# Kernel optimization log

Measured on AMD Instinct MI355X. Metric: run time of the kernel, lower is better.

Reference implementation:

```python
import jax, jax.numpy as jnp
import numpy as np

N_HASHES = 8
Q_ATTN = 128   # q_attn_size == q_cluster_size
K_ATTN = 128   # k_attn_size == k_cluster_size


def _lsh_positions(queries, keys, alpha, beta):
    """XBOX+ asymmetric transform followed by E2LSH hashing; returns sorted
    positions (cluster assignment = contiguous chunks of the sorted order).
    Mirrors torch's no_grad block: outputs are int indices."""
    q_norms = jnp.linalg.norm(queries, axis=-1, keepdims=True)          # [B,S,1]
    k_norms = jnp.linalg.norm(keys, axis=-1, keepdims=True)
    M = jnp.maximum(q_norms.max(axis=1, keepdims=True),
                    k_norms.max(axis=1, keepdims=True))                 # [B,1,1]
    q_ext = jnp.sqrt(jnp.maximum(M ** 2 - q_norms ** 2, 0.0))
    k_ext = jnp.sqrt(jnp.maximum(M ** 2 - k_norms ** 2, 0.0))
    Q = jnp.concatenate([queries, q_ext, jnp.zeros_like(q_ext)], axis=-1)  # [B,S,d+2]
    K = jnp.concatenate([keys, jnp.zeros_like(k_ext), k_ext], axis=-1)
    # E2LSH: (x @ a + b) / r with r = 1; argsort is invariant to the /r rescale
    q_hash = jnp.einsum('bsd,dh->hbs', Q, alpha) + beta[:, None, None]  # [H,B,S]
    k_hash = jnp.einsum('bsd,dh->hbs', K, alpha) + beta[:, None, None]
    return jnp.argsort(q_hash, axis=-1), jnp.argsort(k_hash, axis=-1)


def _smyrf_attention(queries, keys, values, q_pos, k_pos):
    H = q_pos.shape[0]
    bs, q_len, dim = queries.shape
    v_dim = values.shape[-1]
    nc = q_len // Q_ATTN  # num clusters

    def gather(x, pos):  # x: [B,S,D], pos: [H,B,S] -> [H,B,S,D]
        return jnp.take_along_axis(jnp.broadcast_to(x[None], (H,) + x.shape),
                                   pos[..., None], axis=2)

    sq = gather(queries, q_pos).reshape(H, bs, nc, Q_ATTN, dim)
    sk = gather(keys,    k_pos).reshape(H, bs, nc, K_ATTN, dim)
    sv = gather(values,  k_pos).reshape(H, bs, nc, K_ATTN, v_dim)

    # per-cluster attention (norm_factor = 1, matching the torch default)
    inner = jnp.einsum('hbcqd,hbckd->hbcqk', sq, sk)
    lse = jax.nn.logsumexp(inner, axis=-1, keepdims=True)
    dots = jnp.exp(inner - lse)
    bo = jnp.einsum('hbcqk,hbckv->hbcqv', dots, sv).reshape(H, bs, q_len, v_dim)

    # scatter back to original query order
    q_rev = jnp.argsort(q_pos, axis=-1)                                  # [H,B,S]
    o = jnp.take_along_axis(bo, q_rev[..., None], axis=2)                # [H,B,S,V]
    logits = jnp.take_along_axis(lse.reshape(H, bs, q_len), q_rev, axis=2)
    # combine hash rounds: softmax over the hash axis weighted by per-round lse
    probs = jnp.exp(logits - jax.nn.logsumexp(logits, axis=0, keepdims=True))
    return jnp.sum(o * probs[..., None], axis=0)                         # [B,S,V]


def setup_inputs() -> dict:
    key = jax.random.key(0)
    kq, kk, kv, ka, kb = jax.random.split(key, 5)
    bs, seqlen, dim = 16, 4096, 64
    queries = jax.random.normal(kq, (bs, seqlen, dim), dtype=jnp.float32)
    keys = jax.random.normal(kk, (bs, seqlen, dim), dtype=jnp.float32)
    values = jax.random.normal(kv, (bs, seqlen, dim), dtype=jnp.float32)
    alpha = jax.random.normal(ka, (dim + 2, N_HASHES), dtype=jnp.float32)
    beta = jax.random.uniform(kb, (N_HASHES,), dtype=jnp.float32)  # U(0, r=1)
    return {"queries": queries, "keys": keys, "values": values,
            "alpha": alpha, "beta": beta}


def reference(queries, keys, values, alpha, beta):
    q_pos, k_pos = _lsh_positions(queries, keys, alpha, beta)
    return _smyrf_attention(queries, keys, values, q_pos, k_pos)
```

## Files before the change

### kernel.cpp

```cpp
#include <hip/hip_runtime.h>
#include <hip/hip_bf16.h>

#define BS 16
#define SEQ 4096
#define DIM 64
#define NH 8
#define CL 128
#define NC (SEQ/CL)
#define NPAIR (NH*BS)
#define QS2 72
#define VS2 136
#define PS 72

typedef __attribute__((ext_vector_type(8))) short bf8_t;
typedef __attribute__((ext_vector_type(4))) float f4_t;

__device__ __forceinline__ unsigned short f2bf(float x) {
    union { float f; unsigned u; } a; a.f = x;
    unsigned r = a.u + 0x7FFF + ((a.u >> 16) & 1);
    return (unsigned short)(r >> 16);
}
__device__ __forceinline__ float bf2f(unsigned short h) {
    union { unsigned u; float f; } a; a.u = ((unsigned)h) << 16; return a.f;
}
__device__ __forceinline__ void split8(float4 a, float4 b, bf8_t& hi, bf8_t& lo) {
    float v[8] = {a.x, a.y, a.z, a.w, b.x, b.y, b.z, b.w};
    #pragma unroll
    for (int j = 0; j < 8; ++j) {
        unsigned short h = f2bf(v[j]);
        hi[j] = (short)h;
        lo[j] = (short)f2bf(v[j] - bf2f(h));
    }
}

__global__ __launch_bounds__(256) void norms_kernel(const float* __restrict__ q,
        const float* __restrict__ k, float* __restrict__ qn2, float* __restrict__ kn2,
        unsigned int* __restrict__ M2bits) {
    int blk = blockIdx.x;
    const int qblocks = BS*SEQ/64;
    bool is_q = blk < qblocks;
    int rowbase = (is_q ? blk : blk - qblocks) * 64;
    const float* src = is_q ? q : k;
    float* dst = is_q ? qn2 : kn2;
    int t = threadIdx.x;
    int sub = t & 3;
    int r = rowbase + (t >> 2);
    const float4* row4 = (const float4*)(src + (size_t)r*DIM) + sub*4;
    float s = 0.f;
    #pragma unroll
    for (int c2 = 0; c2 < 4; ++c2) {
        float4 vv = row4[c2];
        s += vv.x*vv.x + vv.y*vv.y + vv.z*vv.z + vv.w*vv.w;
    }
    s += __shfl_xor(s, 1);
    s += __shfl_xor(s, 2);
    if (sub == 0) dst[r] = s;
    __shared__ float red[256];
    red[t] = s;
    __syncthreads();
    #pragma unroll
    for (int o = 128; o > 0; o >>= 1) {
        if (t < o) red[t] = fmaxf(red[t], red[t + o]);
        __syncthreads();
    }
    if (t == 0) atomicMax(&M2bits[r / SEQ], __float_as_uint(red[0]));
}

__global__ __launch_bounds__(256) void hash_kernel(const float* __restrict__ q,
        const float* __restrict__ k, const float* __restrict__ qn2,
        const float* __restrict__ kn2, const unsigned int* __restrict__ M2bits,
        const float* __restrict__ alpha, const float* __restrict__ beta,
        float* __restrict__ qh, float* __restrict__ kh) {
    int t = threadIdx.x;
    int sub = t & 3;
    int r = blockIdx.x * 64 + (t >> 2);
    const float4* q4 = (const float4*)(q + (size_t)r*DIM) + sub*4;
    const float4* k4 = (const float4*)(k + (size_t)r*DIM) + sub*4;
    float qa[NH], ka[NH];
    #pragma unroll
    for (int h = 0; h < NH; ++h) { qa[h] = 0.f; ka[h] = 0.f; }
    #pragma unroll
    for (int c2 = 0; c2 < 4; ++c2) {
        int d0 = sub*16 + c2*4;
        float4 qv = q4[c2], kv = k4[c2];
        #pragma unroll
        for (int h = 0; h < NH; ++h) {
            float a0 = alpha[(d0+0)*NH+h], a1 = alpha[(d0+1)*NH+h];
            float a2 = alpha[(d0+2)*NH+h], a3 = alpha[(d0+3)*NH+h];
            qa[h] += qv.x*a0 + qv.y*a1 + qv.z*a2 + qv.w*a3;
            ka[h] += kv.x*a0 + kv.y*a1 + kv.z*a2 + kv.w*a3;
        }
    }
    #pragma unroll
    for (int h = 0; h < NH; ++h) {
        qa[h] += __shfl_xor(qa[h], 1); qa[h] += __shfl_xor(qa[h], 2);
        ka[h] += __shfl_xor(ka[h], 1); ka[h] += __shfl_xor(ka[h], 2);
    }
    if (sub == 0) {
        int b = r / SEQ;
        float m2 = __uint_as_float(M2bits[b]);
        float qe = sqrtf(fmaxf(m2 - qn2[r], 0.f));
        float ke = sqrtf(fmaxf(m2 - kn2[r], 0.f));
        #pragma unroll
        for (int h = 0; h < NH; ++h) {
            qh[(size_t)h*BS*SEQ + r] = qa[h] + qe*alpha[DIM*NH + h] + beta[h];
            kh[(size_t)h*BS*SEQ + r] = ka[h] + ke*alpha[(DIM+1)*NH + h] + beta[h];
        }
    }
}

__global__ __launch_bounds__(512) void sort_kernel(const float* __restrict__ qh,
        const float* __restrict__ kh, int* __restrict__ qpos, int* __restrict__ kpos) {
    __shared__ float sh[SEQ];
    __shared__ int si[SEQ];
    int blk = blockIdx.x;
    const float* src; int* dst;
    if (blk < NPAIR) { src = qh + (size_t)blk*SEQ; dst = qpos + (size_t)blk*SEQ; }
    else { src = kh + (size_t)(blk - NPAIR)*SEQ; dst = kpos + (size_t)(blk - NPAIR)*SEQ; }
    int t = threadIdx.x;
    for (int i = t; i < SEQ; i += 512) { sh[i] = src[i]; si[i] = i; }
    __syncthreads();
    for (int kk = 2; kk <= SEQ; kk <<= 1) {
        for (int j = kk >> 1; j > 0; j >>= 1) {
            #pragma unroll
            for (int w = 0; w < SEQ/512; ++w) {
                int i = t + w*512;
                int ixj = i ^ j;
                if (ixj > i) {
                    bool up = (i & kk) == 0;
                    float h1 = sh[i], h2 = sh[ixj];
                    int i1 = si[i], i2 = si[ixj];
                    bool gt = (h1 > h2) || (h1 == h2 && i1 > i2);
                    if (gt == up) { sh[i] = h2; sh[ixj] = h1; si[i] = i2; si[ixj] = i1; }
                }
            }
            __syncthreads();
        }
    }
    for (int i = t; i < SEQ; i += 512) dst[i] = si[i];
}

__global__ __launch_bounds__(512, 6) void lse_kernel(const float* __restrict__ q,
        const float* __restrict__ k, const int* __restrict__ qpos,
        const int* __restrict__ kpos, float* __restrict__ lse) {
    extern __shared__ char smem[];
    short* khi = (short*)smem;
    short* klo = khi + 128*QS2;
    int* qp = (int*)(smem + 36864);
    int* kp = qp + CL;
    int blk = blockIdx.x;
    int c = blk & (NC-1);
    int hb = blk / NC;
    int b = hb & (BS-1);
    int t = threadIdx.x, lane = t & 63, w = t >> 6;
    int l15 = lane & 15, lg = lane >> 4;
    size_t posbase = (size_t)hb*SEQ + (size_t)c*CL;

    int qrow = qpos[posbase + w*16 + l15];
    const float* qsrc = q + ((size_t)b*SEQ + qrow)*DIM + lg*8;
    float4 qv0 = *(const float4*)(qsrc);
    float4 qv1 = *(const float4*)(qsrc + 4);
    float4 qv2 = *(const float4*)(qsrc + 32);
    float4 qv3 = *(const float4*)(qsrc + 36);

    if (t < CL) qp[t] = qpos[posbase + t];
    else if (t < 2*CL) kp[t - CL] = kpos[posbase + (t - CL)];
    __syncthreads();
    for (int task = t; task < 2048; task += 512) {
        int r = task >> 4, d4 = task & 15;
        float4 vv = ((const float4*)(k + ((size_t)b*SEQ + kp[r])*DIM))[d4];
        ushort4 h, l;
        h.x = f2bf(vv.x); h.y = f2bf(vv.y); h.z = f2bf(vv.z); h.w = f2bf(vv.w);
        l.x = f2bf(vv.x - bf2f(h.x)); l.y = f2bf(vv.y - bf2f(h.y));
        l.z = f2bf(vv.z - bf2f(h.z)); l.w = f2bf(vv.w - bf2f(h.w));
        *(ushort4*)(khi + r*QS2 + d4*4) = h;
        *(ushort4*)(klo + r*QS2 + d4*4) = l;
    }
    bf8_t ah[2], al[2];
    split8(qv0, qv1, ah[0], al[0]);
    split8(qv2, qv3, ah[1], al[1]);
    __syncthreads();
    f4_t acc[8] = {};
    #pragma unroll
    for (int ks = 0; ks < 2; ++ks) {
        #pragma unroll
        for (int ct = 0; ct < 8; ++ct) {
            int brow = (ct*16 + l15)*QS2 + lg*8 + 32*ks;
            bf8_t bh = *(bf8_t*)(khi + brow);
            bf8_t bl = *(bf8_t*)(klo + brow);
            acc[ct] = __builtin_amdgcn_mfma_f32_16x16x32_bf16(ah[ks], bh, acc[ct], 0, 0, 0);
            acc[ct] = __builtin_amdgcn_mfma_f32_16x16x32_bf16(al[ks], bh, acc[ct], 0, 0, 0);
            acc[ct] = __builtin_amdgcn_mfma_f32_16x16x32_bf16(ah[ks], bl, acc[ct], 0, 0, 0);
        }
    }
    #pragma unroll
    for (int r = 0; r < 4; ++r) {
        float m = acc[0][r];
        #pragma unroll
        for (int ct = 1; ct < 8; ++ct) m = fmaxf(m, acc[ct][r]);
        m = fmaxf(m, __shfl_xor(m, 1)); m = fmaxf(m, __shfl_xor(m, 2));
        m = fmaxf(m, __shfl_xor(m, 4)); m = fmaxf(m, __shfl_xor(m, 8));
        float s = 0.f;
        #pragma unroll
        for (int ct = 0; ct < 8; ++ct) s += __expf(acc[ct][r] - m);
        s += __shfl_xor(s, 1); s += __shfl_xor(s, 2);
        s += __shfl_xor(s, 4); s += __shfl_xor(s, 8);
        if (l15 == 0) lse[(size_t)hb*SEQ + qp[w*16 + lg*4 + r]] = m + __logf(s);
    }
}

__global__ __launch_bounds__(256) void z_kernel(const float* __restrict__ lse,
        float* __restrict__ Z) {
    int i = blockIdx.x * 256 + threadIdx.x;
    float vals[NH];
    float m = -1e30f;
    #pragma unroll
    for (int h = 0; h < NH; ++h) {
        vals[h] = lse[(size_t)h*BS*SEQ + i];
        m = fmaxf(m, vals[h]);
    }
    float s = 0.f;
    #pragma unroll
    for (int h = 0; h < NH; ++h) s += expf(vals[h] - m);
    Z[i] = m + logf(s);
}

__global__ __launch_bounds__(512, 6) void attn_kernel(const float* __restrict__ q,
        const float* __restrict__ k, const float* __restrict__ v,
        const int* __restrict__ qpos, const int* __restrict__ kpos,
        const float* __restrict__ Z, float* __restrict__ out) {
    extern __shared__ char smem[];
    short* khi = (short*)smem;
    short* klo = khi + 128*QS2;
    short* vt = (short*)smem;
    short* pb = (short*)(smem + 17408);
    int* qp = (int*)(smem + 36864);
    int* kp = qp + CL;
    float* zq = (float*)(kp + CL);
    int blk = blockIdx.x;
    int c = blk & (NC-1);
    int hb = blk / NC;
    int b = hb & (BS-1);
    int t = threadIdx.x, lane = t & 63, w = t >> 6;
    int l15 = lane & 15, lg = lane >> 4;
    size_t posbase = (size_t)hb*SEQ + (size_t)c*CL;

    int qrow = qpos[posbase + w*16 + l15];
    const float* qsrc = q + ((size_t)b*SEQ + qrow)*DIM + lg*8;
    float4 qv0 = *(const float4*)(qsrc);
    float4 qv1 = *(const float4*)(qsrc + 4);
    float4 qv2 = *(const float4*)(qsrc + 32);
    float4 qv3 = *(const float4*)(qsrc + 36);

    if (t < CL) qp[t] = qpos[posbase + t];
    else if (t < 2*CL) kp[t - CL] = kpos[posbase + (t - CL)];
    __syncthreads();
    if (t < CL) zq[t] = Z[(size_t)b*SEQ + qp[t]];
    for (int task = t; task < 2048; task += 512) {
        int r = task >> 4, d4 = task & 15;
        float4 vv = ((const float4*)(k + ((size_t)b*SEQ + kp[r])*DIM))[d4];
        ushort4 h, l;
        h.x = f2bf(vv.x); h.y = f2bf(vv.y); h.z = f2bf(vv.z); h.w = f2bf(vv.w);
        l.x = f2bf(vv.x - bf2f(h.x)); l.y = f2bf(vv.y - bf2f(h.y));
        l.z = f2bf(vv.z - bf2f(h.z)); l.w = f2bf(vv.w - bf2f(h.w));
        *(ushort4*)(khi + r*QS2 + d4*4) = h;
        *(ushort4*)(klo + r*QS2 + d4*4) = l;
    }
    bf8_t ah[2], al[2];
    split8(qv0, qv1, ah[0], al[0]);
    split8(qv2, qv3, ah[1], al[1]);
    __syncthreads();
    f4_t acc[8] = {};
    #pragma unroll
    for (int ks = 0; ks < 2; ++ks) {
        #pragma unroll
        for (int ct = 0; ct < 8; ++ct) {
            int brow = (ct*16 + l15)*QS2 + lg*8 + 32*ks;
            bf8_t bh = *(bf8_t*)(khi + brow);
            bf8_t bl = *(bf8_t*)(klo + brow);
            acc[ct] = __builtin_amdgcn_mfma_f32_16x16x32_bf16(ah[ks], bh, acc[ct], 0, 0, 0);
            acc[ct] = __builtin_amdgcn_mfma_f32_16x16x32_bf16(al[ks], bh, acc[ct], 0, 0, 0);
            acc[ct] = __builtin_amdgcn_mfma_f32_16x16x32_bf16(ah[ks], bl, acc[ct], 0, 0, 0);
        }
    }
    {
        float zr[4];
        #pragma unroll
        for (int r = 0; r < 4; ++r) zr[r] = zq[w*16 + lg*4 + r];
        #pragma unroll
        for (int ct = 0; ct < 8; ++ct)
            #pragma unroll
            for (int r = 0; r < 4; ++r)
                acc[ct][r] = __expf(acc[ct][r] - zr[r]);
    }
    __syncthreads();
    float vr0[8], vr1[8];
    #pragma unroll
    for (int j = 0; j < 8; ++j) {
        int r0 = kp[w*8 + j];
        int r1 = kp[(w+8)*8 + j];
        vr0[j] = v[((size_t)b*SEQ + r0)*DIM + lane];
        vr1[j] = v[((size_t)b*SEQ + r1)*DIM + lane];
    }
    #pragma unroll
    for (int ct = 0; ct < 4; ++ct)
        #pragma unroll
        for (int r = 0; r < 4; ++r)
            pb[(w*16 + lg*4 + r)*PS + ct*16 + l15] = (short)f2bf(acc[ct][r]);
    {
        bf8_t pk0, pk1;
        #pragma unroll
        for (int j = 0; j < 8; ++j) { pk0[j] = (short)f2bf(vr0[j]); pk1[j] = (short)f2bf(vr1[j]); }
        *(bf8_t*)(vt + lane*VS2 + w*8)     = pk0;
        *(bf8_t*)(vt + lane*VS2 + (w+8)*8) = pk1;
    }
    __syncthreads();
    f4_t oacc[4] = {};
    #pragma unroll
    for (int ks = 0; ks < 2; ++ks) {
        bf8_t pa = *(bf8_t*)(pb + (w*16 + l15)*PS + ks*32 + lg*8);
        #pragma unroll
        for (int n = 0; n < 4; ++n) {
            bf8_t vb = *(bf8_t*)(vt + (n*16 + l15)*VS2 + ks*32 + lg*8);
            oacc[n] = __builtin_amdgcn_mfma_f32_16x16x32_bf16(pa, vb, oacc[n], 0, 0, 0);
        }
    }
    __syncthreads();
    #pragma unroll
    for (int ct = 4; ct < 8; ++ct)
        #pragma unroll
        for (int r = 0; r < 4; ++r)
            pb[(w*16 + lg*4 + r)*PS + (ct-4)*16 + l15] = (short)f2bf(acc[ct][r]);
    __syncthreads();
    #pragma unroll
    for (int ks = 2; ks < 4; ++ks) {
        bf8_t pa = *(bf8_t*)(pb + (w*16 + l15)*PS + (ks-2)*32 + lg*8);
        #pragma unroll
        for (int n = 0; n < 4; ++n) {
            bf8_t vb = *(bf8_t*)(vt + (n*16 + l15)*VS2 + ks*32 + lg*8);
            oacc[n] = __builtin_amdgcn_mfma_f32_16x16x32_bf16(pa, vb, oacc[n], 0, 0, 0);
        }
    }
    #pragma unroll
    for (int n = 0; n < 4; ++n)
        #pragma unroll
        for (int r = 0; r < 4; ++r) {
            int row = w*16 + lg*4 + r;
            atomicAdd(out + ((size_t)b*SEQ + qp[row])*DIM + n*16 + l15, oacc[n][r]);
        }
}

extern "C" void kernel_launch(void* const* d_in, const int* in_sizes, int n_in,
                              void* d_out, int out_size, void* d_ws, size_t ws_size,
                              hipStream_t stream) {
    const float* q     = (const float*)d_in[0];
    const float* k     = (const float*)d_in[1];
    const float* v     = (const float*)d_in[2];
    const float* alpha = (const float*)d_in[3];
    const float* beta  = (const float*)d_in[4];
    float* out = (float*)d_out;

    float* ws   = (float*)d_ws;
    float* M2   = ws;
    float* qn2  = ws + 64;
    float* kn2  = qn2 + BS*SEQ;
    float* qh   = kn2 + BS*SEQ;
    float* kh   = qh + (size_t)NH*BS*SEQ;
    int*   qpos = (int*)(kh + (size_t)NH*BS*SEQ);
    int*   kpos = qpos + (size_t)NH*BS*SEQ;
    float* lse  = (float*)(kpos + (size_t)NH*BS*SEQ);
    float* Z    = lse + (size_t)NH*BS*SEQ;

    hipMemsetAsync(M2, 0, 64*sizeof(float), stream);
    hipMemsetAsync(out, 0, (size_t)out_size*sizeof(float), stream);

    norms_kernel<<<2*BS*SEQ/64, 256, 0, stream>>>(q, k, qn2, kn2, (unsigned int*)M2);
    hash_kernel<<<BS*SEQ/64, 256, 0, stream>>>(q, k, qn2, kn2, (const unsigned int*)M2,
                                               alpha, beta, qh, kh);
    sort_kernel<<<2*NPAIR, 512, 0, stream>>>(qh, kh, qpos, kpos);

    const int lse_lds  = 36864 + 2*CL*(int)sizeof(int);
    const int attn_lds = 36864 + 2*CL*(int)sizeof(int) + CL*(int)sizeof(float);
    lse_kernel<<<NH*BS*NC, 512, lse_lds, stream>>>(q, k, qpos, kpos, lse);
    z_kernel<<<BS*SEQ/256, 256, 0, stream>>>(lse, Z);
    attn_kernel<<<NH*BS*NC, 512, attn_lds, stream>>>(q, k, v, qpos, kpos, Z, out);
}
```

Measured before the change: 392.0 us.

## Bitonic sort: handle small-stride stages in registers with 1024 threads

The bitonic sort kernel now gives each thread 4 contiguous elements and runs the compare-exchange steps with stride below 4 in registers. This removes two shared-memory passes and two barriers per merge stage, plus the initial stages. The block size also doubles to 1024 threads, and loads and stores use vectorised float4/int4 accesses. The larger-stride stages still go through shared memory. The bigger block may limit how many blocks run per CU.

```diff
diff --git a/kernel.cpp b/kernel.cpp
--- a/kernel.cpp
+++ b/kernel.cpp
@@ -109,7 +109,15 @@
     }
 }
 
-__global__ __launch_bounds__(512) void sort_kernel(const float* __restrict__ qh,
+__device__ __forceinline__ void ce(float& h1, int& i1, float& h2, int& i2, bool up) {
+    bool gt = (h1 > h2) || (h1 == h2 && i1 > i2);
+    if (gt == up) {
+        float th = h1; h1 = h2; h2 = th;
+        int ti = i1; i1 = i2; i2 = ti;
+    }
+}
+
+__global__ __launch_bounds__(1024) void sort_kernel(const float* __restrict__ qh,
         const float* __restrict__ kh, int* __restrict__ qpos, int* __restrict__ kpos) {
     __shared__ float sh[SEQ];
     __shared__ int si[SEQ];
@@ -118,16 +126,30 @@
     if (blk < NPAIR) { src = qh + (size_t)blk*SEQ; dst = qpos + (size_t)blk*SEQ; }
     else { src = kh + (size_t)(blk - NPAIR)*SEQ; dst = kpos + (size_t)(blk - NPAIR)*SEQ; }
     int t = threadIdx.x;
-    for (int i = t; i < SEQ; i += 512) { sh[i] = src[i]; si[i] = i; }
-    __syncthreads();
-    for (int kk = 2; kk <= SEQ; kk <<= 1) {
-        for (int j = kk >> 1; j > 0; j >>= 1) {
+    int base = t * 4;
+
+    float4 hv = *(const float4*)(src + base);
+    float h[4] = {hv.x, hv.y, hv.z, hv.w};
+    int id[4] = {base, base + 1, base + 2, base + 3};
+    ce(h[0], id[0], h[1], id[1], true);
+    ce(h[2], id[2], h[3], id[3], false);
+    bool up4 = (base & 4) == 0;
+    ce(h[0], id[0], h[2], id[2], up4);
+    ce(h[1], id[1], h[3], id[3], up4);
+    ce(h[0], id[0], h[1], id[1], up4);
+    ce(h[2], id[2], h[3], id[3], up4);
+    *(float4*)(sh + base) = make_float4(h[0], h[1], h[2], h[3]);
+    *(int4*)(si + base) = make_int4(id[0], id[1], id[2], id[3]);
+    __syncthreads();
+
+    for (int k = 8; k <= SEQ; k <<= 1) {
+        for (int j = k >> 1; j >= 4; j >>= 1) {
             #pragma unroll
-            for (int w = 0; w < SEQ/512; ++w) {
-                int i = t + w*512;
+            for (int w = 0; w < 4; ++w) {
+                int i = t + w * 1024;
                 int ixj = i ^ j;
                 if (ixj > i) {
-                    bool up = (i & kk) == 0;
+                    bool up = (i & k) == 0;
                     float h1 = sh[i], h2 = sh[ixj];
                     int i1 = si[i], i2 = si[ixj];
                     bool gt = (h1 > h2) || (h1 == h2 && i1 > i2);
@@ -136,8 +158,23 @@
             }
             __syncthreads();
         }
-    }
-    for (int i = t; i < SEQ; i += 512) dst[i] = si[i];
+        float4 lh = *(const float4*)(sh + base);
+        int4 li = *(const int4*)(si + base);
+        h[0] = lh.x; h[1] = lh.y; h[2] = lh.z; h[3] = lh.w;
+        id[0] = li.x; id[1] = li.y; id[2] = li.z; id[3] = li.w;
+        bool up = (base & k) == 0;
+        ce(h[0], id[0], h[2], id[2], up);
+        ce(h[1], id[1], h[3], id[3], up);
+        ce(h[0], id[0], h[1], id[1], up);
+        ce(h[2], id[2], h[3], id[3], up);
+        if (k == SEQ) {
+            *(int4*)(dst + base) = make_int4(id[0], id[1], id[2], id[3]);
+        } else {
+            *(float4*)(sh + base) = make_float4(h[0], h[1], h[2], h[3]);
+            *(int4*)(si + base) = make_int4(id[0], id[1], id[2], id[3]);
+            __syncthreads();
+        }
+    }
 }
 
 __global__ __launch_bounds__(512, 6) void lse_kernel(const float* __restrict__ q,
@@ -377,7 +414,7 @@
     norms_kernel<<<2*BS*SEQ/64, 256, 0, stream>>>(q, k, qn2, kn2, (unsigned int*)M2);
     hash_kernel<<<BS*SEQ/64, 256, 0, stream>>>(q, k, qn2, kn2, (const unsigned int*)M2,
                                                alpha, beta, qh, kh);
-    sort_kernel<<<2*NPAIR, 512, 0, stream>>>(qh, kh, qpos, kpos);
+    sort_kernel<<<2*NPAIR, 1024, 0, stream>>>(qh, kh, qpos, kpos);
 
     const int lse_lds  = 36864 + 2*CL*(int)sizeof(int);
     const int attn_lds = 36864 + 2*CL*(int)sizeof(int) + CL*(int)sizeof(float);
```

Result: faster. 369.3 us (-5.8%).
